# Kernel optimization log

Measured on AMD Instinct MI355X. Metric: run time of the kernel, lower is better.

Reference implementation:

```python
import jax, jax.numpy as jnp
import numpy as np

DN = ('NHWC', 'HWIO', 'NHWC')


def setup_inputs() -> dict:
    key = jax.random.key(0)
    ks = jax.random.split(key, 5)
    B, H, W, C = 2, 256, 256, 192
    heads = 4
    x = jax.random.normal(ks[0], (B, H, W, C), dtype=jnp.float32)
    w_qkv = jax.random.normal(ks[1], (1, 1, C, 3 * C), dtype=jnp.float32) * 0.05
    b_qkv = jnp.zeros((3 * C,), dtype=jnp.float32)
    w_dw = jax.random.normal(ks[2], (3, 3, 1, 3 * C), dtype=jnp.float32) * 0.05
    b_dw = jnp.zeros((3 * C,), dtype=jnp.float32)
    temperature = jnp.ones((1, heads, 1, 1), dtype=jnp.float32)
    w_out = jax.random.normal(ks[3], (1, 1, C, C), dtype=jnp.float32) * 0.05
    b_out = jnp.zeros((C,), dtype=jnp.float32)
    return {"x": x, "w_qkv": w_qkv, "b_qkv": b_qkv, "w_dw": w_dw,
            "b_dw": b_dw, "temperature": temperature, "w_out": w_out,
            "b_out": b_out}


def _mdta(x, w_qkv, b_qkv, w_dw, b_dw, temperature, w_out, b_out):
    B, H, W, C = x.shape
    heads = temperature.shape[1]
    c = C // heads  # per-head channels
    # 1x1 pointwise qkv projection -> [B,H,W,3C]
    qkv = jax.lax.conv_general_dilated(x, w_qkv, (1, 1), 'SAME',
                                       dimension_numbers=DN) + b_qkv
    # 3x3 depthwise conv (groups = 3C)
    qkv = jax.lax.conv_general_dilated(qkv, w_dw, (1, 1), 'SAME',
                                       dimension_numbers=DN,
                                       feature_group_count=3 * C) + b_dw
    q, k, v = jnp.split(qkv, 3, axis=-1)  # each [B,H,W,C]

    def to_heads(t):
        # [B,H,W,C] -> [B, heads, c, HW]
        return t.reshape(B, H * W, heads, c).transpose(0, 2, 3, 1)

    q, k, v = to_heads(q), to_heads(k), to_heads(v)
    # L2-normalize along the spatial (HW) axis
    q = q / jnp.maximum(jnp.linalg.norm(q, axis=-1, keepdims=True), 1e-12)
    k = k / jnp.maximum(jnp.linalg.norm(k, axis=-1, keepdims=True), 1e-12)
    # channel-wise transposed attention: [B,heads,c,c]
    attn = jnp.einsum('bhcn,bhdn->bhcd', q, k) * temperature
    attn = jax.nn.softmax(attn, axis=-1)
    out = jnp.einsum('bhcd,bhdn->bhcn', attn, v)  # [B,heads,c,HW]
    out = out.transpose(0, 3, 1, 2).reshape(B, H, W, C)
    # output 1x1 projection
    out = jax.lax.conv_general_dilated(out, w_out, (1, 1), 'SAME',
                                       dimension_numbers=DN) + b_out
    return out


def reference(x, w_qkv, b_qkv, w_dw, b_dw, temperature, w_out, b_out):
    return _mdta(x, w_qkv, b_qkv, w_dw, b_dw, temperature, w_out, b_out)
```

## Files before the change

kernel.cpp:

```cpp
#include <hip/hip_runtime.h>

typedef unsigned short ushort_t;
typedef __attribute__((ext_vector_type(8))) short short8;
typedef __attribute__((ext_vector_type(4))) float f32x4;

#define B_ 2
#define HW_ 65536
#define MTOT_ 131072
#define C_ 192
#define C3_ 576
#define HEADS_ 4
#define CH_ 48

#define OFF_QKV0  ((size_t)0)
#define OFF_QKV1  ((size_t)150994944)
#define OFF_P     OFF_QKV0
#define OFF_BT    ((size_t)301989888)
#define OFF_S     ((size_t)302211072)
#define OFF_NQ    ((size_t)302284800)
#define OFF_NK    ((size_t)302286336)
#define OFF_ATTN  ((size_t)302287872)
#define OFF_MT    ((size_t)302361600)

__device__ __forceinline__ float b2f(ushort_t u) {
    unsigned v = ((unsigned)u) << 16;
    return __builtin_bit_cast(float, v);
}
__device__ __forceinline__ ushort_t f2b(float f) {
    unsigned u = __builtin_bit_cast(unsigned, f);
    u = (u + 0x7fffu + ((u >> 16) & 1u)) >> 16;
    return (ushort_t)u;
}
__device__ __forceinline__ void storev(float* p, float v) { *p = v; }
__device__ __forceinline__ void storev(ushort_t* p, float v) { *p = f2b(v); }

__device__ __forceinline__ void load16(const ushort_t* p, uint4& lo, uint4& hi) {
    lo = *(const uint4*)p;
    hi = *(const uint4*)(p + 8);
}
__device__ __forceinline__ void load16(const float* p, uint4& lo, uint4& hi) {
    float4 a = *(const float4*)p;
    float4 b = *(const float4*)(p + 4);
    float4 c = *(const float4*)(p + 8);
    float4 d = *(const float4*)(p + 12);
    ushort_t o[16];
    o[0]=f2b(a.x); o[1]=f2b(a.y); o[2]=f2b(a.z); o[3]=f2b(a.w);
    o[4]=f2b(b.x); o[5]=f2b(b.y); o[6]=f2b(b.z); o[7]=f2b(b.w);
    o[8]=f2b(c.x); o[9]=f2b(c.y); o[10]=f2b(c.z); o[11]=f2b(c.w);
    o[12]=f2b(d.x); o[13]=f2b(d.y); o[14]=f2b(d.z); o[15]=f2b(d.w);
    lo = *(uint4*)o; hi = *(uint4*)(o + 8);
}

__global__ void k0_transpose(const float* __restrict__ w, ushort_t* __restrict__ bt) {
    int idx = blockIdx.x * 256 + threadIdx.x;
    int n = idx / 192, k = idx - n * 192;
    bt[idx] = f2b(w[k * 576 + n]);
}

template <typename AT, typename OutT>
__global__ __launch_bounds__(256) void gemm_k192(
    const AT* __restrict__ A, int lda, int acol0,
    const ushort_t* __restrict__ BT, int bstride, int ntn,
    const float* __restrict__ bias,
    OutT* __restrict__ Cout, int ldc)
{
    const int per = gridDim.x >> 3;
    const int bid = blockIdx.x;
    const int lb  = (bid & 7) * per + (bid >> 3);
    const int mt  = lb / ntn;
    const int m0  = mt * 64;
    const int n0  = (lb - mt * ntn) * 64;
    const ushort_t* bt = BT + (bstride ? (size_t)(m0 >> 16) * (size_t)bstride : 0);

    __shared__ ushort_t As[64 * 72];
    __shared__ ushort_t Bs[64 * 72];

    const int t = threadIdx.x;
    const int wave = t >> 6, lane = t & 63;
    const int quad = lane >> 4, l15 = lane & 15;
    const int wm = (wave >> 1) * 32, wn = (wave & 1) * 32;
    const int srow = t >> 2, scol = (t & 3) * 16;

    f32x4 acc[2][2] = {};

    for (int kk = 0; kk < 192; kk += 64) {
        const AT* ga = A + (size_t)(m0 + srow) * lda + acol0 + kk + scol;
        uint4 va0, va1;
        load16(ga, va0, va1);
        const ushort_t* gb = bt + (size_t)(n0 + srow) * 192 + kk + scol;
        uint4 vb0 = *(const uint4*)gb;
        uint4 vb1 = *(const uint4*)(gb + 8);
        *(uint4*)&As[srow * 72 + scol] = va0;
        *(uint4*)&As[srow * 72 + scol + 8] = va1;
        *(uint4*)&Bs[srow * 72 + scol] = vb0;
        *(uint4*)&Bs[srow * 72 + scol + 8] = vb1;
        __syncthreads();
#pragma unroll
        for (int ks = 0; ks < 2; ks++) {
            short8 a0 = *(const short8*)&As[(wm + l15) * 72 + ks * 32 + quad * 8];
            short8 a1 = *(const short8*)&As[(wm + 16 + l15) * 72 + ks * 32 + quad * 8];
            short8 b0 = *(const short8*)&Bs[(wn + l15) * 72 + ks * 32 + quad * 8];
            short8 b1 = *(const short8*)&Bs[(wn + 16 + l15) * 72 + ks * 32 + quad * 8];
            acc[0][0] = __builtin_amdgcn_mfma_f32_16x16x32_bf16(a0, b0, acc[0][0], 0, 0, 0);
            acc[0][1] = __builtin_amdgcn_mfma_f32_16x16x32_bf16(a0, b1, acc[0][1], 0, 0, 0);
            acc[1][0] = __builtin_amdgcn_mfma_f32_16x16x32_bf16(a1, b0, acc[1][0], 0, 0, 0);
            acc[1][1] = __builtin_amdgcn_mfma_f32_16x16x32_bf16(a1, b1, acc[1][1], 0, 0, 0);
        }
        __syncthreads();
    }
#pragma unroll
    for (int sm = 0; sm < 2; sm++) {
#pragma unroll
        for (int sn = 0; sn < 2; sn++) {
            int col = n0 + wn + sn * 16 + l15;
            float bv = bias ? bias[col] : 0.f;
#pragma unroll
            for (int r = 0; r < 4; r++) {
                int row = m0 + wm + sm * 16 + quad * 4 + r;
                storev(&Cout[(size_t)row * ldc + col], acc[sm][sn][r] + bv);
            }
        }
    }
}

#define R_STRIP 16

__global__ __launch_bounds__(256) void k2_dwconv(const ushort_t* __restrict__ qkv0,
        const float* __restrict__ wdw, const float* __restrict__ bdw,
        ushort_t* __restrict__ qkv1)
{
    const int tid = blockIdx.x * 256 + threadIdx.x;
    const int c4 = tid % 144;
    const int t1 = tid / 144;
    const int x  = t1 & 255;
    const int t2 = t1 >> 8;
    const int s  = t2 & 15;
    const int b  = t2 >> 4;
    const int y0 = s * R_STRIP;
    const int cbase = c4 * 4;

    const bool xm = (x > 0), xp = (x < 255);
    const ushort_t* colbase = qkv0 + ((size_t)(b * HW_ + x) * C3_ + cbase);
    ushort_t*       ocol    = qkv1 + ((size_t)(b * HW_ + x) * C3_ + cbase);
    const size_t rstride = (size_t)256 * C3_;

    float w[3][3][4], bw[4];
#pragma unroll
    for (int ky = 0; ky < 3; ++ky)
#pragma unroll
        for (int kx = 0; kx < 3; ++kx) {
            float4 wv = *(const float4*)(wdw + ((ky * 3 + kx) * C3_ + cbase));
            w[ky][kx][0] = wv.x; w[ky][kx][1] = wv.y; w[ky][kx][2] = wv.z; w[ky][kx][3] = wv.w;
        }
    {
        float4 bv = *(const float4*)(bdw + cbase);
        bw[0] = bv.x; bw[1] = bv.y; bw[2] = bv.z; bw[3] = bv.w;
    }

    const uint2 z2 = make_uint2(0, 0);
    auto loadrow = [&](int r, uint2& d0, uint2& d1, uint2& d2) {
        if ((unsigned)r <= 255u) {
            const ushort_t* p = colbase + (size_t)r * rstride;
            d1 = *(const uint2*)p;
            d0 = xm ? *(const uint2*)(p - C3_) : z2;
            d2 = xp ? *(const uint2*)(p + C3_) : z2;
        } else { d0 = z2; d1 = z2; d2 = z2; }
    };

    float A[3][4] = {};
    uint2 c0, c1, c2;
    loadrow(y0 - 1, c0, c1, c2);

#pragma unroll
    for (int RR = 0; RR < R_STRIP + 2; ++RR) {
        const int r = y0 - 1 + RR;
        uint2 n0 = z2, n1 = z2, n2 = z2;
        if (RR < R_STRIP + 1) loadrow(r + 1, n0, n1, n2);

        float rf[3][4];
        {
            const ushort_t* dd = (const ushort_t*)&c0;
#pragma unroll
            for (int j = 0; j < 4; ++j) rf[0][j] = b2f(dd[j]);
            dd = (const ushort_t*)&c1;
#pragma unroll
            for (int j = 0; j < 4; ++j) rf[1][j] = b2f(dd[j]);
            dd = (const ushort_t*)&c2;
#pragma unroll
            for (int j = 0; j < 4; ++j) rf[2][j] = b2f(dd[j]);
        }

        if (RR >= 1 && RR <= R_STRIP) {
#pragma unroll
            for (int kx = 0; kx < 3; ++kx)
#pragma unroll
                for (int j = 0; j < 4; ++j)
                    A[RR % 3][j] = fmaf(rf[kx][j], w[1][kx][j], A[RR % 3][j]);
        }
        if (RR <= R_STRIP - 1) {
#pragma unroll
            for (int kx = 0; kx < 3; ++kx)
#pragma unroll
                for (int j = 0; j < 4; ++j)
                    A[(RR + 1) % 3][j] = fmaf(rf[kx][j], w[0][kx][j], A[(RR + 1) % 3][j]);
        }
        if (RR >= 2) {
#pragma unroll
            for (int kx = 0; kx < 3; ++kx)
#pragma unroll
                for (int j = 0; j < 4; ++j)
                    A[(RR + 2) % 3][j] = fmaf(rf[kx][j], w[2][kx][j], A[(RR + 2) % 3][j]);
            ushort_t ov[4];
#pragma unroll
            for (int j = 0; j < 4; ++j) {
                ov[j] = f2b(A[(RR + 2) % 3][j] + bw[j]);
                A[(RR + 2) % 3][j] = 0.f;
            }
            *(uint2*)(ocol + (size_t)(r - 1) * rstride) = *(uint2*)ov;
        }
        c0 = n0; c1 = n1; c2 = n2;
    }
}

#define GR_LDSSTRIDE 136

__global__ __launch_bounds__(256) void k3_gram_mfma(const ushort_t* __restrict__ qkv1,
        float* __restrict__ P)
{
    const int bh = blockIdx.y;
    const int b = bh >> 2, h = bh & 3;
    const int slice = blockIdx.x;
    const int t = threadIdx.x;
    const int wave = t >> 6, lane = t & 63;
    const int quad = lane >> 4, l15 = lane & 15;

    __shared__ float red[7680];
    ushort_t* Z = (ushort_t*)red;

    f32x4 acc[15] = {};
    const ushort_t* basep = qkv1 + (size_t)(b * HW_) * C3_;
    const int row = t & 127;
    const int seghalf = t >> 7;

    for (int tile = 0; tile < 8; ++tile) {
        const int nbase = slice * 1024 + tile * 128;
        uint4 u[6];
#pragma unroll
        for (int k = 0; k < 6; ++k) {
            int seg = k * 2 + seghalf;
            int cg = (seg < 6) ? (h * CH_ + seg * 8) : (C_ + h * CH_ + (seg - 6) * 8);
            u[k] = *(const uint4*)(basep + (size_t)(nbase + row) * C3_ + cg);
        }
        __syncthreads();
#pragma unroll
        for (int k = 0; k < 6; ++k) {
            int seg = k * 2 + seghalf;
            int zc = seg * 8;
            const ushort_t* dd = (const ushort_t*)&u[k];
#pragma unroll
            for (int j = 0; j < 8; ++j)
                Z[(zc + j) * GR_LDSSTRIDE + row] = dd[j];
        }
        __syncthreads();
        const int n0 = wave * 32 + quad * 8;
        short8 F[6];
#pragma unroll
        for (int c = 0; c < 6; ++c)
            F[c] = *(const short8*)&Z[(c * 16 + l15) * GR_LDSSTRIDE + n0];
#pragma unroll
        for (int i = 0; i < 3; ++i)
#pragma unroll
            for (int j = 0; j < 3; ++j)
                acc[i * 3 + j] = __builtin_amdgcn_mfma_f32_16x16x32_bf16(F[i], F[3 + j], acc[i * 3 + j], 0, 0, 0);
#pragma unroll
        for (int i = 0; i < 3; ++i) {
            acc[9 + i]  = __builtin_amdgcn_mfma_f32_16x16x32_bf16(F[i], F[i], acc[9 + i], 0, 0, 0);
            acc[12 + i] = __builtin_amdgcn_mfma_f32_16x16x32_bf16(F[3 + i], F[3 + i], acc[12 + i], 0, 0, 0);
        }
    }

    __syncthreads();
    if (wave & 1) {
        float* dst = red + (wave >> 1) * (15 * 256);
#pragma unroll
        for (int tt = 0; tt < 15; ++tt)
            *(f32x4*)&dst[tt * 256 + lane * 4] = acc[tt];
    }
    __syncthreads();
    if (!(wave & 1)) {
        const float* src = red + (wave >> 1) * (15 * 256);
        const int sp = slice * 2 + (wave >> 1);
#pragma unroll
        for (int tt = 0; tt < 15; ++tt) {
            f32x4 v = *(const f32x4*)&src[tt * 256 + lane * 4];
#pragma unroll
            for (int r = 0; r < 4; ++r) {
                int e = (quad * 4 + r) * 16 + l15;
                P[(((size_t)bh * 15 + tt) * 128 + sp) * 256 + e] = acc[tt][r] + v[r];
            }
        }
    }
}

__global__ __launch_bounds__(256) void k3r_reduce(const float* __restrict__ P,
        float* __restrict__ S, float* __restrict__ NQ, float* __restrict__ NK)
{
    int idx = blockIdx.x * 256 + threadIdx.x;
    int bh = idx / 3840;
    int rem = idx - bh * 3840;
    int tt = rem >> 8;
    int e = rem & 255;
    const float* p = P + (((size_t)bh * 15 + tt) * 128) * 256 + e;
    float s = 0.f;
#pragma unroll 8
    for (int sp = 0; sp < 128; ++sp) s += p[(size_t)sp * 256];
    int r = e >> 4, c = e & 15;
    if (tt < 9) {
        int i = tt / 3, j = tt - i * 3;
        S[bh * 2304 + (i * 16 + r) * 48 + j * 16 + c] = s;
    } else if (tt < 12) {
        if (r == c) NQ[bh * 48 + (tt - 9) * 16 + r] = s;
    } else {
        if (r == c) NK[bh * 48 + (tt - 12) * 16 + r] = s;
    }
}

__global__ void k4a_softmax(const float* __restrict__ S, const float* __restrict__ NQ,
                            const float* __restrict__ NK, const float* __restrict__ temp,
                            float* __restrict__ ATT)
{
    int bh = blockIdx.y, cq = blockIdx.x;
    int h = bh & 3;
    int t = threadIdx.x;
    float nq = fmaxf(sqrtf(NQ[bh * 48 + cq]), 1e-12f);
    float tv = temp[h];
    float logit = -1e30f;
    if (t < 48) {
        float nk = fmaxf(sqrtf(NK[bh * 48 + t]), 1e-12f);
        logit = S[bh * 2304 + cq * 48 + t] * tv / (nq * nk);
    }
    float m = logit;
    for (int o = 32; o > 0; o >>= 1) m = fmaxf(m, __shfl_xor(m, o));
    float e = (t < 48) ? __expf(logit - m) : 0.f;
    float ssum = e;
    for (int o = 32; o > 0; o >>= 1) ssum += __shfl_xor(ssum, o);
    if (t < 48) ATT[bh * 2304 + cq * 48 + t] = e / ssum;
}

__global__ void k4b_buildM(const float* __restrict__ ATT, const float* __restrict__ wout,
                           ushort_t* __restrict__ MT)
{
    int idx = blockIdx.x * 256 + threadIdx.x;
    int b = idx / 36864; int rem = idx - b * 36864;
    int j = rem / 192;   int d = rem - j * 192;
    int h = d / 48, dd = d - h * 48;
    const float* ap = ATT + (size_t)(b * 4 + h) * 2304 + dd;
    const float* wp = wout + (size_t)(h * 48) * 192 + j;
    float s = 0.f;
#pragma unroll 8
    for (int cq = 0; cq < 48; cq++) s += ap[cq * 48] * wp[cq * 192];
    MT[idx] = f2b(s);
}

extern "C" void kernel_launch(void* const* d_in, const int* in_sizes, int n_in,
                              void* d_out, int out_size, void* d_ws, size_t ws_size,
                              hipStream_t stream) {
    const float* x     = (const float*)d_in[0];
    const float* w_qkv = (const float*)d_in[1];
    const float* b_qkv = (const float*)d_in[2];
    const float* w_dw  = (const float*)d_in[3];
    const float* b_dw  = (const float*)d_in[4];
    const float* temp  = (const float*)d_in[5];
    const float* w_out = (const float*)d_in[6];
    const float* b_out = (const float*)d_in[7];
    float* out = (float*)d_out;

    char* ws = (char*)d_ws;
    ushort_t* qkv0 = (ushort_t*)(ws + OFF_QKV0);
    ushort_t* qkv1 = (ushort_t*)(ws + OFF_QKV1);
    float*    Pb   = (float*)(ws + OFF_P);
    ushort_t* btq  = (ushort_t*)(ws + OFF_BT);
    float*    Sb   = (float*)(ws + OFF_S);
    float*    NQ   = (float*)(ws + OFF_NQ);
    float*    NK   = (float*)(ws + OFF_NK);
    float*    ATT  = (float*)(ws + OFF_ATTN);
    ushort_t* MT   = (ushort_t*)(ws + OFF_MT);

    k0_transpose<<<432, 256, 0, stream>>>(w_qkv, btq);
    gemm_k192<float, ushort_t><<<18432, 256, 0, stream>>>(x, 192, 0, btq, 0, 9, b_qkv, qkv0, 576);
    k2_dwconv<<<4608, 256, 0, stream>>>(qkv0, w_dw, b_dw, qkv1);
    k3_gram_mfma<<<dim3(64, 8), 256, 0, stream>>>(qkv1, Pb);
    k3r_reduce<<<120, 256, 0, stream>>>(Pb, Sb, NQ, NK);
    k4a_softmax<<<dim3(48, 8), 64, 0, stream>>>(Sb, NQ, NK, temp, ATT);
    k4b_buildM<<<288, 256, 0, stream>>>(ATT, w_out, MT);
    gemm_k192<ushort_t, float><<<6144, 256, 0, stream>>>(qkv1, 576, 384, MT, 36864, 3, b_out, out, 192);
}
```

Measured before the change: 468.4 us.

## Widen GEMM tile to 64x192 and stage epilogue through LDS for coalesced stores

```diff
diff --git a/kernel.cpp b/kernel.cpp
--- a/kernel.cpp
+++ b/kernel.cpp
@@ -60,20 +60,20 @@
 template <typename AT, typename OutT>
 __global__ __launch_bounds__(256) void gemm_k192(
     const AT* __restrict__ A, int lda, int acol0,
-    const ushort_t* __restrict__ BT, int bstride, int ntn,
+    const ushort_t* __restrict__ BT, int bstride, int stn,
     const float* __restrict__ bias,
     OutT* __restrict__ Cout, int ldc)
 {
     const int per = gridDim.x >> 3;
     const int bid = blockIdx.x;
     const int lb  = (bid & 7) * per + (bid >> 3);
-    const int mt  = lb / ntn;
+    const int mt  = lb / stn;
     const int m0  = mt * 64;
-    const int n0  = (lb - mt * ntn) * 64;
+    const int ns  = (lb - mt * stn) * 192;
     const ushort_t* bt = BT + (bstride ? (size_t)(m0 >> 16) * (size_t)bstride : 0);
 
-    __shared__ ushort_t As[64 * 72];
-    __shared__ ushort_t Bs[64 * 72];
+    __shared__ ushort_t SM[4 * 64 * 72];
+    ushort_t* As = SM;
 
     const int t = threadIdx.x;
     const int wave = t >> 6, lane = t & 63;
@@ -81,45 +81,67 @@
     const int wm = (wave >> 1) * 32, wn = (wave & 1) * 32;
     const int srow = t >> 2, scol = (t & 3) * 16;
 
-    f32x4 acc[2][2] = {};
+    f32x4 acc[3][2][2] = {};
 
     for (int kk = 0; kk < 192; kk += 64) {
-        const AT* ga = A + (size_t)(m0 + srow) * lda + acol0 + kk + scol;
         uint4 va0, va1;
-        load16(ga, va0, va1);
-        const ushort_t* gb = bt + (size_t)(n0 + srow) * 192 + kk + scol;
-        uint4 vb0 = *(const uint4*)gb;
-        uint4 vb1 = *(const uint4*)(gb + 8);
+        load16(A + (size_t)(m0 + srow) * lda + acol0 + kk + scol, va0, va1);
+        uint4 vb[3][2];
+#pragma unroll
+        for (int nt = 0; nt < 3; ++nt) {
+            const ushort_t* gb = bt + (size_t)(ns + nt * 64 + srow) * 192 + kk + scol;
+            vb[nt][0] = *(const uint4*)gb;
+            vb[nt][1] = *(const uint4*)(gb + 8);
+        }
         *(uint4*)&As[srow * 72 + scol] = va0;
         *(uint4*)&As[srow * 72 + scol + 8] = va1;
-        *(uint4*)&Bs[srow * 72 + scol] = vb0;
-        *(uint4*)&Bs[srow * 72 + scol + 8] = vb1;
+#pragma unroll
+        for (int nt = 0; nt < 3; ++nt) {
+            ushort_t* bs = SM + (nt + 1) * 4608;
+            *(uint4*)&bs[srow * 72 + scol] = vb[nt][0];
+            *(uint4*)&bs[srow * 72 + scol + 8] = vb[nt][1];
+        }
         __syncthreads();
 #pragma unroll
         for (int ks = 0; ks < 2; ks++) {
             short8 a0 = *(const short8*)&As[(wm + l15) * 72 + ks * 32 + quad * 8];
             short8 a1 = *(const short8*)&As[(wm + 16 + l15) * 72 + ks * 32 + quad * 8];
-            short8 b0 = *(const short8*)&Bs[(wn + l15) * 72 + ks * 32 + quad * 8];
-            short8 b1 = *(const short8*)&Bs[(wn + 16 + l15) * 72 + ks * 32 + quad * 8];
-            acc[0][0] = __builtin_amdgcn_mfma_f32_16x16x32_bf16(a0, b0, acc[0][0], 0, 0, 0);
-            acc[0][1] = __builtin_amdgcn_mfma_f32_16x16x32_bf16(a0, b1, acc[0][1], 0, 0, 0);
-            acc[1][0] = __builtin_amdgcn_mfma_f32_16x16x32_bf16(a1, b0, acc[1][0], 0, 0, 0);
-            acc[1][1] = __builtin_amdgcn_mfma_f32_16x16x32_bf16(a1, b1, acc[1][1], 0, 0, 0);
+#pragma unroll
+            for (int nt = 0; nt < 3; ++nt) {
+                const ushort_t* bs = SM + (nt + 1) * 4608;
+                short8 b0 = *(const short8*)&bs[(wn + l15) * 72 + ks * 32 + quad * 8];
+                short8 b1 = *(const short8*)&bs[(wn + 16 + l15) * 72 + ks * 32 + quad * 8];
+                acc[nt][0][0] = __builtin_amdgcn_mfma_f32_16x16x32_bf16(a0, b0, acc[nt][0][0], 0, 0, 0);
+                acc[nt][0][1] = __builtin_amdgcn_mfma_f32_16x16x32_bf16(a0, b1, acc[nt][0][1], 0, 0, 0);
+                acc[nt][1][0] = __builtin_amdgcn_mfma_f32_16x16x32_bf16(a1, b0, acc[nt][1][0], 0, 0, 0);
+                acc[nt][1][1] = __builtin_amdgcn_mfma_f32_16x16x32_bf16(a1, b1, acc[nt][1][1], 0, 0, 0);
+            }
         }
         __syncthreads();
     }
-#pragma unroll
-    for (int sm = 0; sm < 2; sm++) {
-#pragma unroll
-        for (int sn = 0; sn < 2; sn++) {
-            int col = n0 + wn + sn * 16 + l15;
-            float bv = bias ? bias[col] : 0.f;
-#pragma unroll
-            for (int r = 0; r < 4; r++) {
-                int row = m0 + wm + sm * 16 + quad * 4 + r;
-                storev(&Cout[(size_t)row * ldc + col], acc[sm][sn][r] + bv);
+
+    OutT* ew = (OutT*)SM + (size_t)wave * 32 * 40;
+    const int erow = lane >> 1, ecol = (lane & 1) * 16;
+    constexpr int EPC = 16 / (int)sizeof(OutT);
+    constexpr int NCH = 16 / EPC;
+#pragma unroll
+    for (int nt = 0; nt < 3; ++nt) {
+        const int n0g = ns + nt * 64;
+#pragma unroll
+        for (int sm = 0; sm < 2; sm++)
+#pragma unroll
+            for (int sn = 0; sn < 2; sn++) {
+                float bv = bias ? bias[n0g + wn + sn * 16 + l15] : 0.f;
+#pragma unroll
+                for (int r = 0; r < 4; r++)
+                    storev(&ew[(sm * 16 + quad * 4 + r) * 40 + sn * 16 + l15],
+                           acc[nt][sm][sn][r] + bv);
             }
-        }
+        const OutT* er = ew + erow * 40 + ecol;
+        OutT* gp = Cout + (size_t)(m0 + wm + erow) * ldc + n0g + wn + ecol;
+#pragma unroll
+        for (int h = 0; h < NCH; ++h)
+            *(uint4*)(gp + h * EPC) = *(const uint4*)(er + h * EPC);
     }
 }
 
@@ -387,11 +409,11 @@
     ushort_t* MT   = (ushort_t*)(ws + OFF_MT);
 
     k0_transpose<<<432, 256, 0, stream>>>(w_qkv, btq);
-    gemm_k192<float, ushort_t><<<18432, 256, 0, stream>>>(x, 192, 0, btq, 0, 9, b_qkv, qkv0, 576);
+    gemm_k192<float, ushort_t><<<6144, 256, 0, stream>>>(x, 192, 0, btq, 0, 3, b_qkv, qkv0, 576);
     k2_dwconv<<<4608, 256, 0, stream>>>(qkv0, w_dw, b_dw, qkv1);
     k3_gram_mfma<<<dim3(64, 8), 256, 0, stream>>>(qkv1, Pb);
     k3r_reduce<<<120, 256, 0, stream>>>(Pb, Sb, NQ, NK);
     k4a_softmax<<<dim3(48, 8), 64, 0, stream>>>(Sb, NQ, NK, temp, ATT);
     k4b_buildM<<<288, 256, 0, stream>>>(ATT, w_out, MT);
-    gemm_k192<ushort_t, float><<<6144, 256, 0, stream>>>(qkv1, 576, 384, MT, 36864, 3, b_out, out, 192);
-}
+    gemm_k192<ushort_t, float><<<2048, 256, 0, stream>>>(qkv1, 576, 384, MT, 36864, 1, b_out, out, 192);
+}
```

Measured after the change: 437.2 us. -6.7%, faster.
